# Kernel optimization log

Hardware: AMD Instinct MI355X
Metric: run time of the kernel (lower is better)

Reference implementation:

```python
import jax, jax.numpy as jnp
import numpy as np

# Dims: B=32 batch, C=64 feat channels, Np=192 priors, No=72 row offsets,
# Ns=36 pooled sample points (maxpool kernel 2), Hd=64 fc hidden.
B, C, Np, No, Hd = 32, 64, 192, 72, 64
NS_POOL = 2  # n_offsets // sample_points
REG_DIM = No + 4  # reg_layers output


def bilinear_sample(feat, gx, gy):
    """torch F.grid_sample(align_corners=True) equivalent for in-range coords.
    feat: [B,C,H,W]; gx,gy: [B,Np,S] normalized to [-1,1]. -> [B,C,Np,S]."""
    Bb, Cc, H, W = feat.shape
    ix = (gx + 1.0) * 0.5 * (W - 1)
    iy = (gy + 1.0) * 0.5 * (H - 1)
    ix0f = jnp.floor(ix); iy0f = jnp.floor(iy)
    wx = ix - ix0f; wy = iy - iy0f
    ix0 = jnp.clip(ix0f.astype(jnp.int32), 0, W - 1)
    iy0 = jnp.clip(iy0f.astype(jnp.int32), 0, H - 1)
    ix1 = jnp.clip(ix0 + 1, 0, W - 1)
    iy1 = jnp.clip(iy0 + 1, 0, H - 1)
    ff = feat.reshape(Bb, Cc, H * W)
    S = gx.shape[1] * gx.shape[2]
    def gather(iy_, ix_):
        idx = (iy_ * W + ix_).reshape(Bb, 1, S)
        g = jnp.take_along_axis(ff, jnp.broadcast_to(idx, (Bb, Cc, S)), axis=2)
        return g.reshape(Bb, Cc, gx.shape[1], gx.shape[2])
    v00 = gather(iy0, ix0); v01 = gather(iy0, ix1)
    v10 = gather(iy1, ix0); v11 = gather(iy1, ix1)
    wx = wx[:, None]; wy = wy[:, None]  # broadcast over C
    return (v00 * (1 - wx) * (1 - wy) + v01 * wx * (1 - wy)
            + v10 * (1 - wx) * wy + v11 * wx * wy)


def _mlp2(h, Ws, bs):
    # two stacked Linear+ReLU layers (num_fc=2)
    for i in range(2):
        h = jax.nn.relu(h @ Ws[i] + bs[i])
    return h


def setup_inputs() -> dict:
    key = jax.random.key(0)
    ks = jax.random.split(key, 24)
    w = lambda k, sh: jax.random.normal(k, sh, dtype=jnp.float32) * 0.05
    return {
        "x0": jax.random.normal(ks[0], (B, C, 40, 100), dtype=jnp.float32),
        "x1": jax.random.normal(ks[1], (B, C, 20, 50), dtype=jnp.float32),
        "x2": jax.random.normal(ks[2], (B, C, 10, 25), dtype=jnp.float32),
        "prior_xs0": jax.random.uniform(ks[3], (Np, No), dtype=jnp.float32),
        "l_weight": w(ks[4], (No,)),              # self.l embedding, sigmoid gate
        "lsgi_w": w(ks[5], (3, C, C)),            # per-stage lsgi projection
        "fc_w": w(ks[6], (C, Hd)), "fc_b": w(ks[7], (Hd,)),
        "cls_w": w(ks[8], (2, Hd, Hd)), "cls_b": w(ks[9], (2, Hd)),
        "cls_ow": w(ks[10], (Hd, 2)), "cls_ob": w(ks[11], (2,)),
        "reg_w": w(ks[12], (2, Hd, Hd)), "reg_b": w(ks[13], (2, Hd)),
        "reg_ow": w(ks[14], (Hd, REG_DIM)), "reg_ob": w(ks[15], (REG_DIM,)),
        "loc_w": w(ks[16], (2, Hd, Hd)), "loc_b": w(ks[17], (2, Hd)),
        "loc_ow": w(ks[18], (Hd, 1)), "loc_ob": w(ks[19], (1,)),
    }


def reference(x0, x1, x2, prior_xs0, l_weight, lsgi_w, fc_w, fc_b,
              cls_w, cls_b, cls_ow, cls_ob, reg_w, reg_b, reg_ow, reg_ob,
              loc_w, loc_b, loc_ow, loc_ob):
    pyramid = [x2, x1, x0]  # reversed: coarsest level first (stage 0)
    prior_feat_ys = jnp.linspace(1.0, 0.0, No, dtype=jnp.float32)
    gy = jnp.broadcast_to((prior_feat_ys * 2.0 - 1.0)[None, None, :], (B, Np, No))
    prior_xs = jnp.broadcast_to(prior_xs0[None], (B, Np, No))
    gate = jax.nn.sigmoid(l_weight)[:, None]  # [No,1]
    stage_feats = []
    outs = []
    for s in range(3):
        gx = prior_xs * 2.0 - 1.0
        pooled = bilinear_sample(pyramid[s], gx, gy)          # [B,C,Np,No]
        pooled = jnp.transpose(pooled, (0, 2, 3, 1)) * gate   # [B,Np,No,C]
        pooled = jax.nn.relu(jnp.einsum('bnoc,cd->bnod', pooled, lsgi_w[s]))
        # MaxPool2d kernel (2,1) over the offset axis -> Ns=36 sample points
        comp = pooled.reshape(B, Np, No // NS_POOL, NS_POOL, C).max(axis=3)
        stage_feats.append(comp)
        # cross-stage fusion (global head): mean over stages and sample points
        fused = jnp.stack(stage_feats, 0).mean(axis=0).mean(axis=2)  # [B,Np,C]
        fc = jax.nn.relu(fused @ fc_w + fc_b)                        # [B,Np,Hd]
        cls = _mlp2(fc, cls_w, cls_b) @ cls_ow + cls_ob              # [B,Np,2]
        reg = _mlp2(fc, reg_w, reg_b) @ reg_ow + reg_ob              # [B,Np,No+4]
        loc = _mlp2(fc, loc_w, loc_b) @ loc_ow + loc_ob              # [B,Np,1]
        outs.append(jnp.concatenate([cls, reg, loc], axis=-1))      # [B,Np,79]
        # refine anchors for next stage from predicted xs
        prior_xs = jax.nn.sigmoid(reg[..., 4:])
    return jnp.stack(outs, axis=0)  # [3,B,Np,79]
```

## Files before the change

### kernel.cpp

```cpp
#include <hip/hip_runtime.h>
#include <hip/hip_bf16.h>

#define Bq   32
#define Cq   64
#define NPq  192
#define NOq  72
#define PTS  (NPq * NOq)
#define REGD 76
#define OUTD 79

typedef __attribute__((ext_vector_type(8))) short short8;
typedef __attribute__((ext_vector_type(4))) float float4v;

__device__ inline unsigned short f2bf(float x) {
    __hip_bfloat16 h = __float2bfloat16(x);
    return *reinterpret_cast<unsigned short*>(&h);
}

__global__ __launch_bounds__(256) void build_tables_kernel(
    const float* __restrict__ f0,
    const float* __restrict__ f1,
    const float* __restrict__ f2,
    const float* __restrict__ lw,
    unsigned short* __restrict__ t0,
    unsigned short* __restrict__ t1,
    unsigned short* __restrict__ t2)
{
    __shared__ float sRow[64 * 101];

    const int tid = threadIdx.x;
    const int o   = blockIdx.x / 96;
    const int sb  = blockIdx.x - o * 96;
    const int s   = sb >> 5;
    const int b   = sb & 31;

    const float* feat; unsigned short* tab; int H, W, SW;
    if (s == 0)      { feat = f0; tab = t0; H = 10; W = 25;  SW = 27;  }
    else if (s == 1) { feat = f1; tab = t1; H = 20; W = 50;  SW = 51;  }
    else             { feat = f2; tab = t2; H = 40; W = 100; SW = 101; }
    const int Wp = W + 1;

    const float ys = 1.0f - (float)o * (1.0f / 71.0f);
    const float iy = ys * (float)(H - 1);
    const float fy = floorf(iy);
    const float wy = iy - fy;
    int iy0 = (int)fy; iy0 = iy0 < 0 ? 0 : (iy0 > H - 1 ? H - 1 : iy0);
    const int iy1 = (iy0 + 1 > H - 1) ? H - 1 : iy0 + 1;
    const float gate = 1.0f / (1.0f + __expf(-lw[o]));

    const float* fb = feat + (size_t)b * 64 * H * W;
    const int iy0W = iy0 * W, iy1W = iy1 * W;

    const int tot = 64 * W;
    for (int idx = tid; idx < tot; idx += 256) {
        const int c = idx / W;
        const int x = idx - c * W;
        const float* f = fb + c * (H * W);
        sRow[c * SW + x] = ((1.0f - wy) * f[iy0W + x] + wy * f[iy1W + x]) * gate;
    }
    __syncthreads();

    unsigned short* to = tab + (size_t)(b * NOq + o) * Wp * 64;
    const int tot2 = Wp * 32;
    for (int idx = tid; idx < tot2; idx += 256) {
        const int x  = idx >> 5;
        const int cp = idx & 31;
        const int xx = (x < W) ? x : (W - 1);
        const float v0 = sRow[(2 * cp)     * SW + xx];
        const float v1 = sRow[(2 * cp + 1) * SW + xx];
        const __hip_bfloat162 h2 = __float22bfloat162_rn(make_float2(v0, v1));
        *(__hip_bfloat162*)(to + x * 64 + 2 * cp) = h2;
    }
}

template<int W>
__global__ __launch_bounds__(256) void fused_pool_head_kernel(
    const unsigned short* __restrict__ tab,
    const float* __restrict__ xsrc, const int xstride,
    const float* __restrict__ lsgi,
    float* __restrict__ sumFeat,
    const int stage,
    const float* __restrict__ fc_w,  const float* __restrict__ fc_b,
    const float* __restrict__ cls_w, const float* __restrict__ cls_b,
    const float* __restrict__ cls_ow, const float* __restrict__ cls_ob,
    const float* __restrict__ reg_w, const float* __restrict__ reg_b,
    const float* __restrict__ reg_ow, const float* __restrict__ reg_ob,
    const float* __restrict__ loc_w, const float* __restrict__ loc_b,
    const float* __restrict__ loc_ow, const float* __restrict__ loc_ob,
    float* __restrict__ out, float* __restrict__ xs_next)
{
    constexpr int Wp = W + 1;
    __shared__ __align__(16) float sF  [8][68];
    __shared__ __align__(16) float bufC[8][64];
    __shared__ __align__(16) float bufA[8][64];
    __shared__ __align__(16) float bufB[8][64];

    const int tid  = threadIdx.x;
    const int w    = tid >> 6;
    const int lane = tid & 63;
    const int ng   = blockIdx.x >> 5;
    const int b    = blockIdx.x & 31;
    const int npair = ng * 4 + w;

    short8 wf[4][2];
    {
        const int kb = ((lane >> 4) & 3) * 8;
        const int dl = lane & 15;
        #pragma unroll
        for (int ks = 0; ks < 2; ++ks)
            #pragma unroll
            for (int dt = 0; dt < 4; ++dt) {
                union { unsigned short u[8]; short8 v; } pk;
                #pragma unroll
                for (int j = 0; j < 8; ++j)
                    pk.u[j] = f2bf(lsgi[(ks * 32 + kb + j) * 64 + dt * 16 + dl]);
                wf[dt][ks] = pk.v;
            }
    }

    const unsigned short* tb = tab + (size_t)b * NOq * Wp * 64;
    const float* xp = xsrc + (size_t)xstride * b;
    const int m  = lane & 15;
    const int kg = lane >> 4;
    const int nt0 = npair * 9;

    float sums0[4] = {0.f, 0.f, 0.f, 0.f};
    float sums1[4] = {0.f, 0.f, 0.f, 0.f};

    #pragma unroll
    for (int ntl = 0; ntl < 9; ++ntl) {
        const int pt = (nt0 + ntl) * 16 + m;
        const int o  = pt % NOq;
        float ixf = xp[pt] * (float)(W - 1);
        ixf = fminf(fmaxf(ixf, 0.0f), (float)(W - 1));
        const float fx = floorf(ixf);
        const float wx = ixf - fx;
        const int ix0 = (int)fx;

        const unsigned short* col = tb + ((size_t)o * Wp + ix0) * 64 + kg * 8;
        const short8 a00 = *(const short8*)(col);
        const short8 a01 = *(const short8*)(col + 64);
        const short8 a10 = *(const short8*)(col + 32);
        const short8 a11 = *(const short8*)(col + 96);

        float wxr[4];
        #pragma unroll
        for (int j = 0; j < 4; ++j) wxr[j] = __shfl(wx, kg * 4 + j);

        const bool hi = (ntl * 16 + (kg * 4)) >= NOq;
        #pragma unroll
        for (int dt = 0; dt < 4; ++dt) {
            float4v c0 = {0.f, 0.f, 0.f, 0.f};
            float4v c1 = {0.f, 0.f, 0.f, 0.f};
            c0 = __builtin_amdgcn_mfma_f32_16x16x32_bf16(a00, wf[dt][0], c0, 0, 0, 0);
            c0 = __builtin_amdgcn_mfma_f32_16x16x32_bf16(a10, wf[dt][1], c0, 0, 0, 0);
            c1 = __builtin_amdgcn_mfma_f32_16x16x32_bf16(a01, wf[dt][0], c1, 0, 0, 0);
            c1 = __builtin_amdgcn_mfma_f32_16x16x32_bf16(a11, wf[dt][1], c1, 0, 0, 0);
            const float v0 = c0[0] + wxr[0] * (c1[0] - c0[0]);
            const float v1 = c0[1] + wxr[1] * (c1[1] - c0[1]);
            const float v2 = c0[2] + wxr[2] * (c1[2] - c0[2]);
            const float v3 = c0[3] + wxr[3] * (c1[3] - c0[3]);
            const float pm0 = fmaxf(fmaxf(v0, v1), 0.f);
            const float pm1 = fmaxf(fmaxf(v2, v3), 0.f);
            const float add = pm0 + pm1;
            if (hi) sums1[dt] += add; else sums0[dt] += add;
        }
    }

    #pragma unroll
    for (int dt = 0; dt < 4; ++dt) {
        float v0 = sums0[dt], v1 = sums1[dt];
        v0 += __shfl_xor(v0, 16); v0 += __shfl_xor(v0, 32);
        v1 += __shfl_xor(v1, 16); v1 += __shfl_xor(v1, 32);
        sums0[dt] = v0; sums1[dt] = v1;
    }

    const float invS = 1.0f / (float)(stage + 1);
    if (lane < 16) {
        const size_t row0 = (size_t)(b * NPq + npair * 2) * 64;
        #pragma unroll
        for (int dt = 0; dt < 4; ++dt) {
            const int d = dt * 16 + lane;
            float t0 = sums0[dt] * (1.0f / 36.0f);
            float t1 = sums1[dt] * (1.0f / 36.0f);
            float* p0 = sumFeat + row0 + d;
            float* p1 = sumFeat + row0 + 64 + d;
            if (stage > 0) { t0 += *p0; t1 += *p1; }
            *p0 = t0; *p1 = t1;
            sF[2 * w][d]     = t0 * invS;
            sF[2 * w + 1][d] = t1 * invS;
        }
    }
    __syncthreads();

    const int pA  = w;
    const int pB  = w + 4;
    const int p0g = b * NPq + ng * 8;

    auto layer = [&](const float* iA, const float* iB, float* oA, float* oB,
                     const float* __restrict__ gw, const float* __restrict__ gb) {
        const float bias = gb[lane];
        float accA = bias, accB = bias;
        #pragma unroll 4
        for (int k = 0; k < 64; k += 4) {
            const float4 a4 = *(const float4*)(iA + k);
            const float4 b4 = *(const float4*)(iB + k);
            const float w0 = gw[(k + 0) * 64 + lane];
            const float w1 = gw[(k + 1) * 64 + lane];
            const float w2 = gw[(k + 2) * 64 + lane];
            const float w3 = gw[(k + 3) * 64 + lane];
            accA += a4.x * w0 + a4.y * w1 + a4.z * w2 + a4.w * w3;
            accB += b4.x * w0 + b4.y * w1 + b4.z * w2 + b4.w * w3;
        }
        oA[lane] = fmaxf(accA, 0.f);
        oB[lane] = fmaxf(accB, 0.f);
        __builtin_amdgcn_wave_barrier();
    };

    layer(sF[pA], sF[pB], bufC[pA], bufC[pB], fc_w, fc_b);

    layer(bufC[pA], bufC[pB], bufA[pA], bufA[pB], cls_w,        cls_b);
    layer(bufA[pA], bufA[pB], bufB[pA], bufB[pB], cls_w + 4096, cls_b + 64);
    {
        const float bA = bufB[pA][lane], bB = bufB[pB][lane];
        const float2 ow = *(const float2*)&cls_ow[lane * 2];
        float v0 = bA * ow.x, v1 = bA * ow.y;
        float v2 = bB * ow.x, v3 = bB * ow.y;
        #pragma unroll
        for (int m2 = 1; m2 < 64; m2 <<= 1) {
            v0 += __shfl_xor(v0, m2);
            v1 += __shfl_xor(v1, m2);
            v2 += __shfl_xor(v2, m2);
            v3 += __shfl_xor(v3, m2);
        }
        if (lane == 0) {
            out[(size_t)(p0g + pA) * OUTD + 0] = v0 + cls_ob[0];
            out[(size_t)(p0g + pA) * OUTD + 1] = v1 + cls_ob[1];
            out[(size_t)(p0g + pB) * OUTD + 0] = v2 + cls_ob[0];
            out[(size_t)(p0g + pB) * OUTD + 1] = v3 + cls_ob[1];
        }
    }

    layer(bufC[pA], bufC[pB], bufA[pA], bufA[pB], reg_w,        reg_b);
    layer(bufA[pA], bufA[pB], bufB[pA], bufB[pB], reg_w + 4096, reg_b + 64);
    {
        const int j1 = lane;
        const int j2 = (lane < 12) ? 64 + lane : 75;
        float zA1 = reg_ob[j1], zB1 = zA1;
        float zA2 = reg_ob[j2], zB2 = zA2;
        #pragma unroll 4
        for (int k = 0; k < 64; k += 4) {
            const float4 a4 = *(const float4*)&bufB[pA][k];
            const float4 b4 = *(const float4*)&bufB[pB][k];
            const float u0 = reg_ow[(k + 0) * REGD + j1];
            const float u1 = reg_ow[(k + 1) * REGD + j1];
            const float u2 = reg_ow[(k + 2) * REGD + j1];
            const float u3 = reg_ow[(k + 3) * REGD + j1];
            const float t0 = reg_ow[(k + 0) * REGD + j2];
            const float t1 = reg_ow[(k + 1) * REGD + j2];
            const float t2 = reg_ow[(k + 2) * REGD + j2];
            const float t3 = reg_ow[(k + 3) * REGD + j2];
            zA1 += a4.x * u0 + a4.y * u1 + a4.z * u2 + a4.w * u3;
            zB1 += b4.x * u0 + b4.y * u1 + b4.z * u2 + b4.w * u3;
            zA2 += a4.x * t0 + a4.y * t1 + a4.z * t2 + a4.w * t3;
            zB2 += b4.x * t0 + b4.y * t1 + b4.z * t2 + b4.w * t3;
        }
        float* orA = out + (size_t)(p0g + pA) * OUTD;
        float* orB = out + (size_t)(p0g + pB) * OUTD;
        float* xsA = xs_next + (size_t)(p0g + pA) * NOq;
        float* xsB = xs_next + (size_t)(p0g + pB) * NOq;
        orA[2 + j1] = zA1;
        orB[2 + j1] = zB1;
        if (lane >= 4) {
            xsA[j1 - 4] = 1.0f / (1.0f + __expf(-zA1));
            xsB[j1 - 4] = 1.0f / (1.0f + __expf(-zB1));
        }
        if (lane < 12) {
            orA[2 + j2] = zA2;
            orB[2 + j2] = zB2;
            xsA[j2 - 4] = 1.0f / (1.0f + __expf(-zA2));
            xsB[j2 - 4] = 1.0f / (1.0f + __expf(-zB2));
        }
    }

    layer(bufC[pA], bufC[pB], bufA[pA], bufA[pB], loc_w,        loc_b);
    layer(bufA[pA], bufA[pB], bufB[pA], bufB[pB], loc_w + 4096, loc_b + 64);
    {
        float v0 = bufB[pA][lane] * loc_ow[lane];
        float v1 = bufB[pB][lane] * loc_ow[lane];
        #pragma unroll
        for (int m2 = 1; m2 < 64; m2 <<= 1) {
            v0 += __shfl_xor(v0, m2);
            v1 += __shfl_xor(v1, m2);
        }
        if (lane == 0) {
            out[(size_t)(p0g + pA) * OUTD + 78] = v0 + loc_ob[0];
            out[(size_t)(p0g + pB) * OUTD + 78] = v1 + loc_ob[0];
        }
    }
}

extern "C" void kernel_launch(void* const* d_in, const int* in_sizes, int n_in,
                              void* d_out, int out_size, void* d_ws, size_t ws_size,
                              hipStream_t stream)
{
    const float* x0        = (const float*)d_in[0];
    const float* x1        = (const float*)d_in[1];
    const float* x2        = (const float*)d_in[2];
    const float* prior_xs0 = (const float*)d_in[3];
    const float* l_weight  = (const float*)d_in[4];
    const float* lsgi_w    = (const float*)d_in[5];
    const float* fc_w      = (const float*)d_in[6];
    const float* fc_b      = (const float*)d_in[7];
    const float* cls_w     = (const float*)d_in[8];
    const float* cls_b     = (const float*)d_in[9];
    const float* cls_ow    = (const float*)d_in[10];
    const float* cls_ob    = (const float*)d_in[11];
    const float* reg_w     = (const float*)d_in[12];
    const float* reg_b     = (const float*)d_in[13];
    const float* reg_ow    = (const float*)d_in[14];
    const float* reg_ob    = (const float*)d_in[15];
    const float* loc_w     = (const float*)d_in[16];
    const float* loc_b     = (const float*)d_in[17];
    const float* loc_ow    = (const float*)d_in[18];
    const float* loc_ob    = (const float*)d_in[19];

    float* out     = (float*)d_out;
    float* sumFeat = (float*)d_ws;
    float* xs      = sumFeat + (size_t)Bq * NPq * Cq;
    unsigned short* tab0 = (unsigned short*)(xs + (size_t)Bq * PTS);
    unsigned short* tab1 = tab0 + (size_t)Bq * NOq * 26  * 64;
    unsigned short* tab2 = tab1 + (size_t)Bq * NOq * 51  * 64;

    hipLaunchKernelGGL(build_tables_kernel, dim3(3 * Bq * NOq), dim3(256), 0, stream,
                       x2, x1, x0, l_weight, tab0, tab1, tab2);

    for (int s = 0; s < 3; ++s) {
        const float* xsrc = (s == 0) ? prior_xs0 : xs;
        const int xstr    = (s == 0) ? 0 : PTS;
        const unsigned short* tb = (s == 0) ? tab0 : (s == 1) ? tab1 : tab2;
        float* outS = out + (size_t)s * Bq * NPq * OUTD;
        if (s == 0)
            hipLaunchKernelGGL((fused_pool_head_kernel<25>), dim3(Bq * 24), dim3(256), 0, stream,
                               tb, xsrc, xstr, lsgi_w + s * 4096, sumFeat, s,
                               fc_w, fc_b, cls_w, cls_b, cls_ow, cls_ob,
                               reg_w, reg_b, reg_ow, reg_ob,
                               loc_w, loc_b, loc_ow, loc_ob, outS, xs);
        else if (s == 1)
            hipLaunchKernelGGL((fused_pool_head_kernel<50>), dim3(Bq * 24), dim3(256), 0, stream,
                               tb, xsrc, xstr, lsgi_w + s * 4096, sumFeat, s,
                               fc_w, fc_b, cls_w, cls_b, cls_ow, cls_ob,
                               reg_w, reg_b, reg_ow, reg_ob,
                               loc_w, loc_b, loc_ow, loc_ob, outS, xs);
        else
            hipLaunchKernelGGL((fused_pool_head_kernel<100>), dim3(Bq * 24), dim3(256), 0, stream,
                               tb, xsrc, xstr, lsgi_w + s * 4096, sumFeat, s,
                               fc_w, fc_b, cls_w, cls_b, cls_ow, cls_ob,
                               reg_w, reg_b, reg_ow, reg_ob,
                               loc_w, loc_b, loc_ow, loc_ob, outS, xs);
    }
}
```

Before: 246.4 us.

## Store raw bf16 feature rows and do vertical interpolation and gating inside MFMA kernel

The precompute kernel no longer builds per-offset rows that are already interpolated vertically and gated, 72 rows per batch and stage. It now only converts the raw H feature rows to the padded bf16 layout. The fused pool kernel gathers two rows, runs twice as many MFMAs and applies the y-interpolation and sigmoid gate in registers, using per-offset tables held in shared memory. This shrinks the table build and its memory footprint, at the cost of doubling the gather loads and matrix work in the main kernel.

```diff
diff --git a/kernel.cpp b/kernel.cpp
--- a/kernel.cpp
+++ b/kernel.cpp
@@ -17,11 +17,10 @@
     return *reinterpret_cast<unsigned short*>(&h);
 }
 
-__global__ __launch_bounds__(256) void build_tables_kernel(
+__global__ __launch_bounds__(256) void build_raw_kernel(
     const float* __restrict__ f0,
     const float* __restrict__ f1,
     const float* __restrict__ f2,
-    const float* __restrict__ lw,
     unsigned short* __restrict__ t0,
     unsigned short* __restrict__ t1,
     unsigned short* __restrict__ t2)
@@ -29,42 +28,30 @@
     __shared__ float sRow[64 * 101];
 
     const int tid = threadIdx.x;
-    const int o   = blockIdx.x / 96;
-    const int sb  = blockIdx.x - o * 96;
-    const int s   = sb >> 5;
-    const int b   = sb & 31;
-
-    const float* feat; unsigned short* tab; int H, W, SW;
-    if (s == 0)      { feat = f0; tab = t0; H = 10; W = 25;  SW = 27;  }
-    else if (s == 1) { feat = f1; tab = t1; H = 20; W = 50;  SW = 51;  }
-    else             { feat = f2; tab = t2; H = 40; W = 100; SW = 101; }
+    int idx = blockIdx.x;
+
+    const float* feat; unsigned short* tab; int H, W, SW, b, y;
+    if (idx < 320)       { feat = f0; tab = t0; H = 10; W = 25;  SW = 27;
+                           b = idx / 10;  y = idx - b * 10; }
+    else if (idx < 960)  { idx -= 320; feat = f1; tab = t1; H = 20; W = 50;  SW = 51;
+                           b = idx / 20;  y = idx - b * 20; }
+    else                 { idx -= 960; feat = f2; tab = t2; H = 40; W = 100; SW = 101;
+                           b = idx / 40;  y = idx - b * 40; }
     const int Wp = W + 1;
 
-    const float ys = 1.0f - (float)o * (1.0f / 71.0f);
-    const float iy = ys * (float)(H - 1);
-    const float fy = floorf(iy);
-    const float wy = iy - fy;
-    int iy0 = (int)fy; iy0 = iy0 < 0 ? 0 : (iy0 > H - 1 ? H - 1 : iy0);
-    const int iy1 = (iy0 + 1 > H - 1) ? H - 1 : iy0 + 1;
-    const float gate = 1.0f / (1.0f + __expf(-lw[o]));
-
-    const float* fb = feat + (size_t)b * 64 * H * W;
-    const int iy0W = iy0 * W, iy1W = iy1 * W;
-
     const int tot = 64 * W;
-    for (int idx = tid; idx < tot; idx += 256) {
-        const int c = idx / W;
-        const int x = idx - c * W;
-        const float* f = fb + c * (H * W);
-        sRow[c * SW + x] = ((1.0f - wy) * f[iy0W + x] + wy * f[iy1W + x]) * gate;
+    for (int i = tid; i < tot; i += 256) {
+        const int c = i / W;
+        const int x = i - c * W;
+        sRow[c * SW + x] = feat[((size_t)(b * 64 + c) * H + y) * W + x];
     }
     __syncthreads();
 
-    unsigned short* to = tab + (size_t)(b * NOq + o) * Wp * 64;
+    unsigned short* to = tab + ((size_t)b * H + y) * Wp * 64;
     const int tot2 = Wp * 32;
-    for (int idx = tid; idx < tot2; idx += 256) {
-        const int x  = idx >> 5;
-        const int cp = idx & 31;
+    for (int i = tid; i < tot2; i += 256) {
+        const int x  = i >> 5;
+        const int cp = i & 31;
         const int xx = (x < W) ? x : (W - 1);
         const float v0 = sRow[(2 * cp)     * SW + xx];
         const float v1 = sRow[(2 * cp + 1) * SW + xx];
@@ -73,10 +60,11 @@
     }
 }
 
-template<int W>
+template<int W, int H>
 __global__ __launch_bounds__(256) void fused_pool_head_kernel(
     const unsigned short* __restrict__ tab,
     const float* __restrict__ xsrc, const int xstride,
+    const float* __restrict__ lw,
     const float* __restrict__ lsgi,
     float* __restrict__ sumFeat,
     const int stage,
@@ -94,6 +82,10 @@
     __shared__ __align__(16) float bufC[8][64];
     __shared__ __align__(16) float bufA[8][64];
     __shared__ __align__(16) float bufB[8][64];
+    __shared__ int   sOff0[72];
+    __shared__ int   sOff1[72];
+    __shared__ float sWyA [72];
+    __shared__ float sGate[72];
 
     const int tid  = threadIdx.x;
     const int w    = tid >> 6;
@@ -101,6 +93,18 @@
     const int ng   = blockIdx.x >> 5;
     const int b    = blockIdx.x & 31;
     const int npair = ng * 4 + w;
+
+    if (tid < 72) {
+        const float ys = 1.0f - (float)tid * (1.0f / 71.0f);
+        const float iy = ys * (float)(H - 1);
+        const float fy = floorf(iy);
+        int iy0 = (int)fy; iy0 = iy0 < 0 ? 0 : (iy0 > H - 1 ? H - 1 : iy0);
+        const int iy1 = (iy0 + 1 > H - 1) ? H - 1 : iy0 + 1;
+        sOff0[tid] = iy0 * (Wp * 64);
+        sOff1[tid] = iy1 * (Wp * 64);
+        sWyA [tid] = iy - fy;
+        sGate[tid] = 1.0f / (1.0f + __expf(-lw[tid]));
+    }
 
     short8 wf[4][2];
     {
@@ -117,8 +121,9 @@
                 wf[dt][ks] = pk.v;
             }
     }
-
-    const unsigned short* tb = tab + (size_t)b * NOq * Wp * 64;
+    __syncthreads();
+
+    const unsigned short* tb = tab + (size_t)b * H * Wp * 64;
     const float* xp = xsrc + (size_t)xstride * b;
     const int m  = lane & 15;
     const int kg = lane >> 4;
@@ -137,31 +142,53 @@
         const float wx = ixf - fx;
         const int ix0 = (int)fx;
 
-        const unsigned short* col = tb + ((size_t)o * Wp + ix0) * 64 + kg * 8;
-        const short8 a00 = *(const short8*)(col);
-        const short8 a01 = *(const short8*)(col + 64);
-        const short8 a10 = *(const short8*)(col + 32);
-        const short8 a11 = *(const short8*)(col + 96);
-
-        float wxr[4];
-        #pragma unroll
-        for (int j = 0; j < 4; ++j) wxr[j] = __shfl(wx, kg * 4 + j);
+        const int xoff = ix0 * 64 + kg * 8;
+        const unsigned short* c0p = tb + sOff0[o] + xoff;
+        const unsigned short* c1p = tb + sOff1[o] + xoff;
+        const short8 a00 = *(const short8*)(c0p);
+        const short8 a01 = *(const short8*)(c0p + 64);
+        const short8 a10 = *(const short8*)(c0p + 32);
+        const short8 a11 = *(const short8*)(c0p + 96);
+        const short8 b00 = *(const short8*)(c1p);
+        const short8 b01 = *(const short8*)(c1p + 64);
+        const short8 b10 = *(const short8*)(c1p + 32);
+        const short8 b11 = *(const short8*)(c1p + 96);
+
+        const float wy_l = sWyA[o];
+        const float g_l  = sGate[o];
+
+        float wxr[4], wyr[4], gr[4];
+        #pragma unroll
+        for (int j = 0; j < 4; ++j) {
+            wxr[j] = __shfl(wx,   kg * 4 + j);
+            wyr[j] = __shfl(wy_l, kg * 4 + j);
+            gr [j] = __shfl(g_l,  kg * 4 + j);
+        }
 
         const bool hi = (ntl * 16 + (kg * 4)) >= NOq;
         #pragma unroll
         for (int dt = 0; dt < 4; ++dt) {
-            float4v c0 = {0.f, 0.f, 0.f, 0.f};
-            float4v c1 = {0.f, 0.f, 0.f, 0.f};
-            c0 = __builtin_amdgcn_mfma_f32_16x16x32_bf16(a00, wf[dt][0], c0, 0, 0, 0);
-            c0 = __builtin_amdgcn_mfma_f32_16x16x32_bf16(a10, wf[dt][1], c0, 0, 0, 0);
-            c1 = __builtin_amdgcn_mfma_f32_16x16x32_bf16(a01, wf[dt][0], c1, 0, 0, 0);
-            c1 = __builtin_amdgcn_mfma_f32_16x16x32_bf16(a11, wf[dt][1], c1, 0, 0, 0);
-            const float v0 = c0[0] + wxr[0] * (c1[0] - c0[0]);
-            const float v1 = c0[1] + wxr[1] * (c1[1] - c0[1]);
-            const float v2 = c0[2] + wxr[2] * (c1[2] - c0[2]);
-            const float v3 = c0[3] + wxr[3] * (c1[3] - c0[3]);
-            const float pm0 = fmaxf(fmaxf(v0, v1), 0.f);
-            const float pm1 = fmaxf(fmaxf(v2, v3), 0.f);
+            float4v cx0y0 = {0.f, 0.f, 0.f, 0.f};
+            float4v cx1y0 = {0.f, 0.f, 0.f, 0.f};
+            float4v cx0y1 = {0.f, 0.f, 0.f, 0.f};
+            float4v cx1y1 = {0.f, 0.f, 0.f, 0.f};
+            cx0y0 = __builtin_amdgcn_mfma_f32_16x16x32_bf16(a00, wf[dt][0], cx0y0, 0, 0, 0);
+            cx0y0 = __builtin_amdgcn_mfma_f32_16x16x32_bf16(a10, wf[dt][1], cx0y0, 0, 0, 0);
+            cx1y0 = __builtin_amdgcn_mfma_f32_16x16x32_bf16(a01, wf[dt][0], cx1y0, 0, 0, 0);
+            cx1y0 = __builtin_amdgcn_mfma_f32_16x16x32_bf16(a11, wf[dt][1], cx1y0, 0, 0, 0);
+            cx0y1 = __builtin_amdgcn_mfma_f32_16x16x32_bf16(b00, wf[dt][0], cx0y1, 0, 0, 0);
+            cx0y1 = __builtin_amdgcn_mfma_f32_16x16x32_bf16(b10, wf[dt][1], cx0y1, 0, 0, 0);
+            cx1y1 = __builtin_amdgcn_mfma_f32_16x16x32_bf16(b01, wf[dt][0], cx1y1, 0, 0, 0);
+            cx1y1 = __builtin_amdgcn_mfma_f32_16x16x32_bf16(b11, wf[dt][1], cx1y1, 0, 0, 0);
+            float v[4];
+            #pragma unroll
+            for (int j = 0; j < 4; ++j) {
+                const float vy0 = cx0y0[j] + wxr[j] * (cx1y0[j] - cx0y0[j]);
+                const float vy1 = cx0y1[j] + wxr[j] * (cx1y1[j] - cx0y1[j]);
+                v[j] = (vy0 + wyr[j] * (vy1 - vy0)) * gr[j];
+            }
+            const float pm0 = fmaxf(fmaxf(v[0], v[1]), 0.f);
+            const float pm1 = fmaxf(fmaxf(v[2], v[3]), 0.f);
             const float add = pm0 + pm1;
             if (hi) sums1[dt] += add; else sums0[dt] += add;
         }
@@ -329,11 +356,11 @@
     float* sumFeat = (float*)d_ws;
     float* xs      = sumFeat + (size_t)Bq * NPq * Cq;
     unsigned short* tab0 = (unsigned short*)(xs + (size_t)Bq * PTS);
-    unsigned short* tab1 = tab0 + (size_t)Bq * NOq * 26  * 64;
-    unsigned short* tab2 = tab1 + (size_t)Bq * NOq * 51  * 64;
-
-    hipLaunchKernelGGL(build_tables_kernel, dim3(3 * Bq * NOq), dim3(256), 0, stream,
-                       x2, x1, x0, l_weight, tab0, tab1, tab2);
+    unsigned short* tab1 = tab0 + (size_t)Bq * 10 * 26  * 64;
+    unsigned short* tab2 = tab1 + (size_t)Bq * 20 * 51  * 64;
+
+    hipLaunchKernelGGL(build_raw_kernel, dim3(2240), dim3(256), 0, stream,
+                       x2, x1, x0, tab0, tab1, tab2);
 
     for (int s = 0; s < 3; ++s) {
         const float* xsrc = (s == 0) ? prior_xs0 : xs;
@@ -341,20 +368,20 @@
         const unsigned short* tb = (s == 0) ? tab0 : (s == 1) ? tab1 : tab2;
         float* outS = out + (size_t)s * Bq * NPq * OUTD;
         if (s == 0)
-            hipLaunchKernelGGL((fused_pool_head_kernel<25>), dim3(Bq * 24), dim3(256), 0, stream,
-                               tb, xsrc, xstr, lsgi_w + s * 4096, sumFeat, s,
+            hipLaunchKernelGGL((fused_pool_head_kernel<25, 10>), dim3(Bq * 24), dim3(256), 0, stream,
+                               tb, xsrc, xstr, l_weight, lsgi_w + s * 4096, sumFeat, s,
                                fc_w, fc_b, cls_w, cls_b, cls_ow, cls_ob,
                                reg_w, reg_b, reg_ow, reg_ob,
                                loc_w, loc_b, loc_ow, loc_ob, outS, xs);
         else if (s == 1)
-            hipLaunchKernelGGL((fused_pool_head_kernel<50>), dim3(Bq * 24), dim3(256), 0, stream,
-                               tb, xsrc, xstr, lsgi_w + s * 4096, sumFeat, s,
+            hipLaunchKernelGGL((fused_pool_head_kernel<50, 20>), dim3(Bq * 24), dim3(256), 0, stream,
+                               tb, xsrc, xstr, l_weight, lsgi_w + s * 4096, sumFeat, s,
                                fc_w, fc_b, cls_w, cls_b, cls_ow, cls_ob,
                                reg_w, reg_b, reg_ow, reg_ob,
                                loc_w, loc_b, loc_ow, loc_ob, outS, xs);
         else
-            hipLaunchKernelGGL((fused_pool_head_kernel<100>), dim3(Bq * 24), dim3(256), 0, stream,
-                               tb, xsrc, xstr, lsgi_w + s * 4096, sumFeat, s,
+            hipLaunchKernelGGL((fused_pool_head_kernel<100, 40>), dim3(Bq * 24), dim3(256), 0, stream,
+                               tb, xsrc, xstr, l_weight, lsgi_w + s * 4096, sumFeat, s,
                                fc_w, fc_b, cls_w, cls_b, cls_ow, cls_ob,
                                reg_w, reg_b, reg_ow, reg_ob,
                                loc_w, loc_b, loc_ow, loc_ob, outS, xs);
```

Measured after the change: 307.1 us. +24.6%, slower.
